# Performance work log

Hardware: AMD Instinct MI355X
Metric: run time of the kernel (lower is better)

## Reference

```python
import jax, jax.numpy as jnp
import numpy as np

N = 6144
M_VID = 1024
M_AUD = 128
APPERTURE = 20
EPS = 1e-6


def setup_inputs() -> dict:
    key = jax.random.key(0)
    ks = jax.random.split(key, 16)
    s = 0.02
    inp = {
        "x": jax.random.normal(ks[0], (1, N, M_VID), dtype=jnp.float32),
        "x_audio": jax.random.normal(ks[1], (1, N, M_AUD), dtype=jnp.float32),
        "seq_len": N,
        "audio_len": N,
        # video self-attention (torch Linear convention: W is [out, in])
        "Wk_v": jax.random.normal(ks[2], (M_VID, M_VID), dtype=jnp.float32) * s,
        "Wq_v": jax.random.normal(ks[3], (M_VID, M_VID), dtype=jnp.float32) * s,
        "Wv_v": jax.random.normal(ks[4], (M_VID, M_VID), dtype=jnp.float32) * s,
        "Wo_v": jax.random.normal(ks[5], (M_VID, M_VID), dtype=jnp.float32) * s,
        # audio self-attention
        "Wk_a": jax.random.normal(ks[6], (M_AUD, M_AUD), dtype=jnp.float32) * s,
        "Wq_a": jax.random.normal(ks[7], (M_AUD, M_AUD), dtype=jnp.float32) * s,
        "Wv_a": jax.random.normal(ks[8], (M_AUD, M_AUD), dtype=jnp.float32) * s,
        "Wo_a": jax.random.normal(ks[9], (M_AUD, M_AUD), dtype=jnp.float32) * s,
        # MLP head
        "ka_w": jax.random.normal(ks[10], (1024, M_VID + M_AUD), dtype=jnp.float32) * s,
        "ka_b": jnp.zeros((1024,), dtype=jnp.float32),
        "kd_w": jax.random.normal(ks[11], (1, 1024), dtype=jnp.float32) * s,
        "kd_b": jnp.zeros((1,), dtype=jnp.float32),
        # layer norms
        "ln_y_g": jnp.ones((M_VID,), dtype=jnp.float32),
        "ln_y_b": jnp.zeros((M_VID,), dtype=jnp.float32),
        "ln_ya_g": jnp.ones((M_AUD,), dtype=jnp.float32),
        "ln_ya_b": jnp.zeros((M_AUD,), dtype=jnp.float32),
        "ln_ka_g": jnp.ones((1024,), dtype=jnp.float32),
        "ln_ka_b": jnp.zeros((1024,), dtype=jnp.float32),
    }
    return inp


def _layer_norm(x, g, b):
    mu = jnp.mean(x, axis=-1, keepdims=True)
    var = jnp.mean((x - mu) ** 2, axis=-1, keepdims=True)
    return (x - mu) / jnp.sqrt(var + EPS) * g + b


def _self_attention(x, Wk, Wq, Wv, Wo):
    # x: [N, d]
    n = x.shape[0]
    K = x @ Wk.T
    Q = (x @ Wq.T) * 0.06
    V = x @ Wv.T
    logits = Q @ K.T  # [N, N]
    # keep only |i-j| < apperture (trimask masks |i-j| >= apperture)
    idx = jnp.arange(n)
    band = jnp.abs(idx[:, None] - idx[None, :]) < APPERTURE
    logits = jnp.where(band, logits, -jnp.inf)
    att = jax.nn.softmax(logits, axis=-1)  # [N, N]
    # torch: y = (V^T @ att)^T == att^T @ V  (note the transpose on att!)
    y = att.T @ V
    return y @ Wo.T, att


def reference(x, x_audio, seq_len, audio_len,
              Wk_v, Wq_v, Wv_v, Wo_v,
              Wk_a, Wq_a, Wv_a, Wo_a,
              ka_w, ka_b, kd_w, kd_b,
              ln_y_g, ln_y_b, ln_ya_g, ln_ya_b, ln_ka_g, ln_ka_b):
    m = x.shape[2]
    m_audio = x_audio.shape[2]
    xf = x.reshape(-1, m)            # [N, 1024]
    xa = x_audio.reshape(-1, m_audio)  # [N, 128]

    y, att_w = _self_attention(xf, Wk_v, Wq_v, Wv_v, Wo_v)
    y = _layer_norm(y + xf, ln_y_g, ln_y_b)

    ya, att_wa = _self_attention(xa, Wk_a, Wq_a, Wv_a, Wo_a)
    ya = _layer_norm(ya + xa, ln_ya_g, ln_ya_b)

    y_comb = jnp.concatenate((y, ya), axis=1)        # [N, 1152]
    att_comb = jnp.concatenate((att_w, att_wa), axis=1)  # [N, 2N]

    h = jax.nn.relu(y_comb @ ka_w.T + ka_b)
    h = _layer_norm(h, ln_ka_g, ln_ka_b)
    score = jax.nn.sigmoid(h @ kd_w.T + kd_b)  # [N, 1]
    score = score.reshape(1, -1)               # [1, N]
    return score, att_comb
```

## Files before the change

kernel.cpp:

```cpp
#include <hip/hip_runtime.h>
#include <stdint.h>

typedef unsigned short u16;
typedef unsigned int u32;
typedef __attribute__((ext_vector_type(8))) short bf16x8;
typedef __attribute__((ext_vector_type(4))) short s16x4;
typedef __attribute__((ext_vector_type(4))) float f32x4;
typedef __attribute__((ext_vector_type(2))) float f32x2;

#define DEV __device__ __forceinline__

DEV u16 f2bf(float f) {
  union { float f; unsigned u; } v; v.f = f;
  unsigned r = v.u + 0x7fffu + ((v.u >> 16) & 1u);
  return (u16)(r >> 16);
}
DEV float bf2f(u16 h) {
  union { u32 u; float f; } v; v.u = ((u32)h) << 16; return v.f;
}
DEV float lo16(u32 w) { union { u32 u; float f; } v; v.u = w << 16; return v.f; }
DEV float hi16(u32 w) { union { u32 u; float f; } v; v.u = w & 0xFFFF0000u; return v.f; }
DEV int imax(int a, int b) { return a > b ? a : b; }
DEV int imin(int a, int b) { return a < b ? a : b; }

DEV int xcd_swz(int b0, int nwg) {
  int q = nwg >> 3, r = nwg & 7, x = b0 & 7, l = b0 >> 3;
  return (x < r ? x * (q + 1) : r * (q + 1) + (x - r) * q) + l;
}

DEV void g2lds16(const u16* g, u16* l) {
  __builtin_amdgcn_global_load_lds(
      (const __attribute__((address_space(1))) void*)g,
      (__attribute__((address_space(3))) void*)l, 16, 0, 0);
}

#define NSEG 5
struct CastTab {
  const float* src[NSEG];
  u16* dst[NSEG];
  int start[NSEG + 1];
};
struct TransTab {
  const float* src[6];
  u16* dst[6];
  int n[6];
  int start[7];
};

__global__ __launch_bounds__(256) void vas_prep(CastTab t, int total4,
                                                int castBlocks, TransTab tt) {
  if ((int)blockIdx.x < castBlocks) {
    int idx = blockIdx.x * 256 + threadIdx.x;
    if (idx >= total4) return;
    int s = 0;
#pragma unroll
    for (int k = 1; k < NSEG; ++k)
      if (idx >= t.start[k]) s = k;
    int local = idx - t.start[s];
    f32x4 f = ((const f32x4*)t.src[s])[local];
    s16x4 o;
    o.x = (short)f2bf(f.x);
    o.y = (short)f2bf(f.y);
    o.z = (short)f2bf(f.z);
    o.w = (short)f2bf(f.w);
    ((s16x4*)t.dst[s])[local] = o;
  } else {
    __shared__ float tl[32][33];
    int b = blockIdx.x - castBlocks;
    int s = 0;
#pragma unroll
    for (int k = 1; k < 6; ++k)
      if (b >= tt.start[k]) s = k;
    b -= tt.start[s];
    const float* src = tt.src[s];
    u16* dst = tt.dst[s];
    const int n = tt.n[s];
    const int tpr = n >> 5;
    const int tr = (b / tpr) * 32, tc = (b % tpr) * 32;
    const int lx = threadIdx.x & 31, ly = threadIdx.x >> 5;
#pragma unroll
    for (int r = 0; r < 4; ++r)
      tl[ly + r * 8][lx] = src[(size_t)(tr + ly + r * 8) * n + tc + lx];
    __syncthreads();
#pragma unroll
    for (int r = 0; r < 4; ++r)
      dst[(size_t)(tc + ly + r * 8) * n + tr + lx] = f2bf(tl[lx][ly + r * 8]);
  }
}

struct GemmP {
  const u16* A;
  const u16* W;
  void* C;
  const float* bias;
  int M, Nn, K, mode;
};

__global__ __launch_bounds__(256) void vas_gemm4(
    GemmP p0, GemmP p1, GemmP p2, GemmP p3, int s1, int s2, int s3) {
  const int bs = xcd_swz(blockIdx.x, gridDim.x);

  GemmP p;
  int bid;
  if (bs < s1) { p = p0; bid = bs; }
  else if (bs < s2) { p = p1; bid = bs - s1; }
  else if (bs < s3) { p = p2; bid = bs - s2; }
  else { p = p3; bid = bs - s3; }

  __shared__ u16 As[2][128 * 32];
  __shared__ u16 Ws[2][128 * 32];
  const int tid = threadIdx.x;
  const int lane = tid & 63;
  const int wave = tid >> 6;

  const int Mb = p.M >> 7, Nb = p.Nn >> 7;
  const int GM = 8;
  int per = GM * Nb;
  int g = bid / per;
  int rem = bid - g * per;
  int gm = imin(GM, Mb - g * GM);
  int mblk = g * GM + rem % gm;
  int nblk = rem / gm;
  const int m0 = mblk * 128;
  const int n0 = nblk * 128;
  const int wm = (wave >> 1) * 64;
  const int wn = (wave & 1) * 64;

  const int smat = wave >> 1;
  const int skh = wave & 1;
  const u16* ssrc = smat ? p.W : p.A;
  const int sbase = smat ? n0 : m0;
  u16* sdstBase = (smat ? &Ws[skh][0] : &As[skh][0]) + lane * 8;
  const int srow = lane >> 2;
  const int scol = (lane & 3) * 8;

  f32x4 acc[4][4] = {};

  for (int k0 = 0; k0 < p.K; k0 += 64) {
#pragma unroll
    for (int u = 0; u < 8; ++u) {
      int r0 = u * 16;
      g2lds16(ssrc + (size_t)(sbase + r0 + srow) * p.K + (k0 + skh * 32 + scol),
              sdstBase + r0 * 32);
    }
    __syncthreads();
#pragma unroll
    for (int kk = 0; kk < 2; ++kk) {
      bf16x8 af[4], bfr[4];
#pragma unroll
      for (int t = 0; t < 4; ++t)
        af[t] = *(const bf16x8*)(&As[kk][0] + (wm + t * 16 + (lane & 15)) * 32 + (lane >> 4) * 8);
#pragma unroll
      for (int t = 0; t < 4; ++t)
        bfr[t] = *(const bf16x8*)(&Ws[kk][0] + (wn + t * 16 + (lane & 15)) * 32 + (lane >> 4) * 8);
#pragma unroll
      for (int mi = 0; mi < 4; ++mi)
#pragma unroll
        for (int ni = 0; ni < 4; ++ni)
          acc[mi][ni] = __builtin_amdgcn_mfma_f32_16x16x32_bf16(af[mi], bfr[ni], acc[mi][ni], 0, 0, 0);
    }
    __syncthreads();
  }

#pragma unroll
  for (int mi = 0; mi < 4; ++mi) {
#pragma unroll
    for (int ni = 0; ni < 4; ++ni) {
      int col = n0 + wn + ni * 16 + (lane & 15);
      float bv = p.bias ? p.bias[col] : 0.f;
#pragma unroll
      for (int r = 0; r < 4; ++r) {
        int row = m0 + wm + mi * 16 + (lane >> 4) * 4 + r;
        float vv = acc[mi][ni][r] + bv;
        size_t idx = (size_t)row * p.Nn + col;
        if (p.mode == 0) ((float*)p.C)[idx] = vv;
        else if (p.mode == 1) ((u16*)p.C)[idx] = f2bf(fmaxf(vv, 0.f));
        else ((u16*)p.C)[idx] = f2bf(vv);
      }
    }
  }
}

__global__ __launch_bounds__(256) void vas_battn(
    const u16* __restrict__ Xv, const u16* __restrict__ Xa,
    const u16* __restrict__ KKVv, const u16* __restrict__ KKVa,
    float* __restrict__ bandV, float* __restrict__ bandA,
    float* __restrict__ attBase, int N, float scale, int vb) {
  const int lane = threadIdx.x & 63;
  const int wave = threadIdx.x >> 6;
  const bool video = blockIdx.x < (u32)vb;
  const int i = (video ? blockIdx.x : blockIdx.x - vb) * 4 + wave;
  const int lo = imax(i - 19, 0);
  const int hi = imin(i + 19, N - 1);
  const int nj = hi - lo + 1;
  float logit = 0.f;
  __shared__ float a_sh[4][40];

  if (video) {
    float qf[16];
    const u16* qrow = Xv + (size_t)i * 1024;
#pragma unroll
    for (int c = 0; c < 2; ++c) {
      bf16x8 qv = *(const bf16x8*)(qrow + c * 512 + lane * 8);
      const u32* qw = (const u32*)&qv;
#pragma unroll
      for (int t = 0; t < 4; ++t) {
        qf[c * 8 + 2 * t] = lo16(qw[t]);
        qf[c * 8 + 2 * t + 1] = hi16(qw[t]);
      }
    }
#pragma unroll 2
    for (int s = 0; s < nj; ++s) {
      const u16* kr = KKVv + (size_t)(lo + s) * 2048;
      float p = 0.f;
#pragma unroll
      for (int c = 0; c < 2; ++c) {
        bf16x8 kv = *(const bf16x8*)(kr + c * 512 + lane * 8);
        const u32* kw = (const u32*)&kv;
#pragma unroll
        for (int t = 0; t < 4; ++t)
          p += lo16(kw[t]) * qf[c * 8 + 2 * t] + hi16(kw[t]) * qf[c * 8 + 2 * t + 1];
      }
#pragma unroll
      for (int off = 32; off; off >>= 1) p += __shfl_xor(p, off);
      if (lane == s) logit = p;
    }
  } else {
    u32 q = *(const u32*)(Xa + (size_t)i * 128 + lane * 2);
    float q0 = lo16(q), q1 = hi16(q);
#pragma unroll 2
    for (int s = 0; s < nj; ++s) {
      u32 k = *(const u32*)(KKVa + (size_t)(lo + s) * 256 + lane * 2);
      float p = lo16(k) * q0 + hi16(k) * q1;
#pragma unroll
      for (int off = 32; off; off >>= 1) p += __shfl_xor(p, off);
      if (lane == s) logit = p;
    }
  }

  logit *= scale;
  float v = (lane < nj) ? logit : -3.4e38f;
  float mx = v;
#pragma unroll
  for (int off = 32; off; off >>= 1) mx = fmaxf(mx, __shfl_xor(mx, off));
  float e = (lane < nj) ? __expf(v - mx) : 0.f;
  float den = e;
#pragma unroll
  for (int off = 32; off; off >>= 1) den += __shfl_xor(den, off);
  float att = (lane < nj) ? e / den : 0.f;
  float* band = video ? bandV : bandA;
  if (lane < 40) {
    band[i * 40 + lane] = att;
    a_sh[wave][lane] = att;
  }

  f32x4* rowp = (f32x4*)(attBase + (size_t)i * 2 * N + (video ? 0 : N));
  const int nchunks = N / 4;
  const int cLo = lo >> 2, cHi = hi >> 2;
  for (int c = lane; c < nchunks; c += 64) {
    f32x4 o = {0.f, 0.f, 0.f, 0.f};
    if (c >= cLo && c <= cHi) {
      int col0 = c * 4;
#pragma unroll
      for (int e2 = 0; e2 < 4; ++e2) {
        int col = col0 + e2;
        if (col >= lo && col <= hi) o[e2] = a_sh[wave][col - lo];
      }
    }
    __builtin_nontemporal_store(o, &rowp[c]);
  }
}

#define JT 8
__global__ __launch_bounds__(256) void vas_apply_ln(
    const u16* __restrict__ KKVv, const u16* __restrict__ KKVa,
    const float* __restrict__ bandV, const float* __restrict__ bandA,
    const float* __restrict__ Xv, const float* __restrict__ Xa,
    const float* __restrict__ gv, const float* __restrict__ bv_,
    const float* __restrict__ ga, const float* __restrict__ ba,
    u16* __restrict__ out, int outStride, int N, int vb) {
  const int tid = threadIdx.x;
  __shared__ float a_sh[(JT + 38) * JT];
  __shared__ float red[2][JT][4];

  if (blockIdx.x < (u32)vb) {
    const int j0 = blockIdx.x * JT;
    const int base = j0 - 19;
    for (int idx = tid; idx < (JT + 38) * JT; idx += 256) {
      int s = idx / JT, jj = idx % JT;
      int i = base + s;
      int j = j0 + jj;
      float w = 0.f;
      if (i >= 0 && i < N) {
        int d = j - i;
        if (d > -20 && d < 20) w = bandV[i * 40 + (j - imax(i - 19, 0))];
      }
      a_sh[s * JT + jj] = w;
    }
    __syncthreads();

    f32x4 acc[JT] = {};
    const int sLo = imax(0, -base);
    const int sHi = imin(JT + 38, N - base);
    s16x4 nxt = *(const s16x4*)(KKVv + (size_t)(base + sLo) * 2048 + 1024 + tid * 4);
    for (int s = sLo; s < sHi; ++s) {
      s16x4 raw = nxt;
      if (s + 1 < sHi)
        nxt = *(const s16x4*)(KKVv + (size_t)(base + s + 1) * 2048 + 1024 + tid * 4);
      f32x4 vv;
      vv.x = bf2f((u16)raw.x);
      vv.y = bf2f((u16)raw.y);
      vv.z = bf2f((u16)raw.z);
      vv.w = bf2f((u16)raw.w);
#pragma unroll
      for (int jj = 0; jj < JT; ++jj) {
        float a = a_sh[s * JT + jj];
        acc[jj].x += a * vv.x;
        acc[jj].y += a * vv.y;
        acc[jj].z += a * vv.z;
        acc[jj].w += a * vv.w;
      }
    }

    const int lane = tid & 63, wave = tid >> 6;
#pragma unroll
    for (int jj = 0; jj < JT; ++jj) {
      f32x4 x4 = ((const f32x4*)(Xv + (size_t)(j0 + jj) * 1024))[tid];
      f32x4 v;
      v.x = acc[jj].x + x4.x;
      v.y = acc[jj].y + x4.y;
      v.z = acc[jj].z + x4.z;
      v.w = acc[jj].w + x4.w;
      acc[jj] = v;
      float s = v.x + v.y + v.z + v.w;
      float s2 = v.x * v.x + v.y * v.y + v.z * v.z + v.w * v.w;
#pragma unroll
      for (int off = 32; off; off >>= 1) {
        s += __shfl_xor(s, off);
        s2 += __shfl_xor(s2, off);
      }
      if (lane == 0) { red[0][jj][wave] = s; red[1][jj][wave] = s2; }
    }
    __syncthreads();
    f32x4 gg = ((const f32x4*)gv)[tid];
    f32x4 bb = ((const f32x4*)bv_)[tid];
#pragma unroll
    for (int jj = 0; jj < JT; ++jj) {
      float S = red[0][jj][0] + red[0][jj][1] + red[0][jj][2] + red[0][jj][3];
      float S2 = red[1][jj][0] + red[1][jj][1] + red[1][jj][2] + red[1][jj][3];
      float mu = S / 1024.f;
      float var = S2 / 1024.f - mu * mu;
      float inv = rsqrtf(var + 1e-6f);
      f32x4 v = acc[jj];
      s16x4 o;
      o.x = (short)f2bf((v.x - mu) * inv * gg.x + bb.x);
      o.y = (short)f2bf((v.y - mu) * inv * gg.y + bb.y);
      o.z = (short)f2bf((v.z - mu) * inv * gg.z + bb.z);
      o.w = (short)f2bf((v.w - mu) * inv * gg.w + bb.w);
      *(s16x4*)(out + (size_t)(j0 + jj) * outStride + tid * 4) = o;
    }
  } else {
    const int lane = tid & 63;
    const int wave = tid >> 6;
    const int j = (blockIdx.x - vb) * 4 + wave;
    const int lo = imax(j - 19, 0);
    const int hi = imin(j + 19, N - 1);
    const int ni = hi - lo + 1;
    float* aw = a_sh + wave * 40;
    if (lane < ni) {
      int i = lo + lane;
      aw[lane] = bandA[i * 40 + (j - imax(i - 19, 0))];
    }
    __syncthreads();
    f32x2 acc = {0.f, 0.f};
#pragma unroll 4
    for (int s = 0; s < ni; ++s) {
      float a = aw[s];
      u32 k = *(const u32*)(KKVa + (size_t)(lo + s) * 256 + 128 + lane * 2);
      acc.x += a * lo16(k);
      acc.y += a * hi16(k);
    }
    f32x2 x2 = *(const f32x2*)(Xa + (size_t)j * 128 + lane * 2);
    float vx = acc.x + x2.x;
    float vy = acc.y + x2.y;
    float s = vx + vy, s2 = vx * vx + vy * vy;
#pragma unroll
    for (int off = 32; off; off >>= 1) {
      s += __shfl_xor(s, off);
      s2 += __shfl_xor(s2, off);
    }
    float mu = s / 128.f;
    float var = s2 / 128.f - mu * mu;
    float inv = rsqrtf(var + 1e-6f);
    f32x2 g2 = *(const f32x2*)(ga + lane * 2);
    f32x2 b2 = *(const f32x2*)(ba + lane * 2);
    u32 o = (u32)f2bf((vx - mu) * inv * g2.x + b2.x) |
            ((u32)f2bf((vy - mu) * inv * g2.y + b2.y) << 16);
    *(u32*)(out + (size_t)j * outStride + 1024 + lane * 2) = o;
  }
}

__global__ __launch_bounds__(256) void vas_head(
    const u16* __restrict__ H, const float* __restrict__ g,
    const float* __restrict__ bb, const float* __restrict__ kw,
    const float* __restrict__ kb, float* __restrict__ score) {
  const int row = blockIdx.x;
  const int tid = threadIdx.x, lane = tid & 63, wave = tid >> 6;
  __shared__ float shA[4], shB[4];
  s16x4 raw = ((const s16x4*)(H + (size_t)row * 1024))[tid];
  f32x4 v;
  v.x = bf2f((u16)raw.x);
  v.y = bf2f((u16)raw.y);
  v.z = bf2f((u16)raw.z);
  v.w = bf2f((u16)raw.w);
  float s = v.x + v.y + v.z + v.w;
  float s2 = v.x * v.x + v.y * v.y + v.z * v.z + v.w * v.w;
#pragma unroll
  for (int off = 32; off; off >>= 1) {
    s += __shfl_xor(s, off);
    s2 += __shfl_xor(s2, off);
  }
  if (lane == 0) { shA[wave] = s; shB[wave] = s2; }
  __syncthreads();
  float S = shA[0] + shA[1] + shA[2] + shA[3];
  float S2 = shB[0] + shB[1] + shB[2] + shB[3];
  float mu = S / 1024.f;
  float var = S2 / 1024.f - mu * mu;
  float inv = rsqrtf(var + 1e-6f);
  f32x4 gg = ((const f32x4*)g)[tid];
  f32x4 bv = ((const f32x4*)bb)[tid];
  f32x4 kv = ((const f32x4*)kw)[tid];
  float p = ((v.x - mu) * inv * gg.x + bv.x) * kv.x +
            ((v.y - mu) * inv * gg.y + bv.y) * kv.y +
            ((v.z - mu) * inv * gg.z + bv.z) * kv.z +
            ((v.w - mu) * inv * gg.w + bv.w) * kv.w;
#pragma unroll
  for (int off = 32; off; off >>= 1) p += __shfl_xor(p, off);
  __syncthreads();
  if (lane == 0) shA[wave] = p;
  __syncthreads();
  if (tid == 0) {
    float P = shA[0] + shA[1] + shA[2] + shA[3] + kb[0];
    score[row] = 1.f / (1.f + __expf(-P));
  }
}

extern "C" void kernel_launch(void* const* d_in, const int* in_sizes, int n_in,
                              void* d_out, int out_size, void* d_ws, size_t ws_size,
                              hipStream_t stream) {
  const float* x = (const float*)d_in[0];
  const float* xa = (const float*)d_in[1];
  const float* Wk_v = (const float*)d_in[4];
  const float* Wq_v = (const float*)d_in[5];
  const float* Wv_v = (const float*)d_in[6];
  const float* Wo_v = (const float*)d_in[7];
  const float* Wk_a = (const float*)d_in[8];
  const float* Wq_a = (const float*)d_in[9];
  const float* Wv_a = (const float*)d_in[10];
  const float* Wo_a = (const float*)d_in[11];
  const float* ka_w = (const float*)d_in[12];
  const float* ka_b = (const float*)d_in[13];
  const float* kd_w = (const float*)d_in[14];
  const float* kd_b = (const float*)d_in[15];
  const float* ln_y_g = (const float*)d_in[16];
  const float* ln_y_b = (const float*)d_in[17];
  const float* ln_ya_g = (const float*)d_in[18];
  const float* ln_ya_b = (const float*)d_in[19];
  const float* ln_ka_g = (const float*)d_in[20];
  const float* ln_ka_b = (const float*)d_in[21];

  const int N = in_sizes[0] / 1024;
  const int MV = 1024, MA = 128, MH = 1152;

  char* wsb = (char*)d_ws;
  size_t off = 0;
  auto alloc = [&](size_t bytes) -> void* {
    void* p = wsb + off;
    off += (bytes + 255) & ~(size_t)255;
    return p;
  };
  u16* xf_b   = (u16*)alloc((size_t)N * MV * 2);
  u16* xa_b   = (u16*)alloc((size_t)N * MA * 2);
  u16* wov_b  = (u16*)alloc((size_t)MV * MV * 2);
  u16* woa_b  = (u16*)alloc((size_t)MA * MA * 2);
  u16* wqTv   = (u16*)alloc((size_t)MV * MV * 2);
  u16* wkTv   = (u16*)alloc((size_t)MV * MV * 2);
  u16* wvTv   = (u16*)alloc((size_t)MV * MV * 2);
  u16* wqTa   = (u16*)alloc((size_t)MA * MA * 2);
  u16* wkTa   = (u16*)alloc((size_t)MA * MA * 2);
  u16* wvTa   = (u16*)alloc((size_t)MA * MA * 2);
  u16* wWv    = (u16*)alloc((size_t)2 * MV * MV * 2);
  u16* wWa    = (u16*)alloc((size_t)2 * MA * MA * 2);
  u16* kaw_b  = (u16*)alloc((size_t)1024 * MH * 2);
  u16* KKVv   = (u16*)alloc((size_t)N * 2 * MV * 2);
  u16* KKVa   = (u16*)alloc((size_t)N * 2 * MA * 2);
  float* bandV = (float*)alloc((size_t)N * 40 * 4);
  float* bandA = (float*)alloc((size_t)N * 40 * 4);
  u16* ycomb_b = (u16*)alloc((size_t)N * MH * 2);
  u16* h_b = (u16*)alloc((size_t)N * 1024 * 2);

  float* dout = (float*)d_out;
  float* attBase = dout + N;

  {
    CastTab t;
    int c = 0, cum = 0;
    auto seg = [&](const float* s, u16* d, size_t n) {
      t.src[c] = s; t.dst[c] = d; t.start[c] = cum; cum += (int)(n / 4); ++c;
    };
    seg(x, xf_b, (size_t)N * MV);
    seg(xa, xa_b, (size_t)N * MA);
    seg(Wo_v, wov_b, (size_t)MV * MV);
    seg(Wo_a, woa_b, (size_t)MA * MA);
    seg(ka_w, kaw_b, (size_t)1024 * MH);
    t.start[c] = cum;
    int castBlocks = (cum + 255) / 256;

    TransTab tt;
    int c2 = 0, cum2 = 0;
    auto seg2 = [&](const float* s, u16* d, int n) {
      tt.src[c2] = s; tt.dst[c2] = d; tt.n[c2] = n; tt.start[c2] = cum2;
      cum2 += (n / 32) * (n / 32); ++c2;
    };
    seg2(Wq_v, wqTv, MV);
    seg2(Wk_v, wkTv, MV);
    seg2(Wv_v, wvTv, MV);
    seg2(Wq_a, wqTa, MA);
    seg2(Wk_a, wkTa, MA);
    seg2(Wv_a, wvTa, MA);
    tt.start[c2] = cum2;

    vas_prep<<<castBlocks + cum2, 256, 0, stream>>>(t, cum, castBlocks, tt);
  }

  {
    GemmP gv = {wqTv, wkTv, wWv, nullptr, MV, MV, MV, 2};
    GemmP uv = {wov_b, wvTv, wWv + (size_t)MV * MV, nullptr, MV, MV, MV, 2};
    GemmP ga = {wqTa, wkTa, wWa, nullptr, MA, MA, MA, 2};
    GemmP ua = {woa_b, wvTa, wWa + (size_t)MA * MA, nullptr, MA, MA, MA, 2};
    int bg = (MV / 128) * (MV / 128);
    vas_gemm4<<<2 * bg + 2, 256, 0, stream>>>(gv, uv, ga, ua, bg, 2 * bg, 2 * bg + 1);
  }

  {
    GemmP pv = {xf_b, wWv, KKVv, nullptr, N, 2 * MV, MV, 2};
    GemmP pa = {xa_b, wWa, KKVa, nullptr, N, 2 * MA, MA, 2};
    int bv = (N / 128) * (2 * MV / 128);
    int ba = (N / 128) * (2 * MA / 128);
    vas_gemm4<<<bv + ba, 256, 0, stream>>>(pv, pa, pa, pa, bv, bv + ba, bv + ba);
  }

  vas_battn<<<N / 2, 256, 0, stream>>>(xf_b, xa_b, KKVv, KKVa, bandV, bandA,
                                       attBase, N, 0.06f, N / 4);

  vas_apply_ln<<<N / JT + N / 4, 256, 0, stream>>>(
      KKVv, KKVa, bandV, bandA, x, xa,
      ln_y_g, ln_y_b, ln_ya_g, ln_ya_b, ycomb_b, MH, N, N / JT);

  {
    GemmP ph = {ycomb_b, kaw_b, h_b, ka_b, N, 1024, MH, 1};
    int bh = (N / 128) * (1024 / 128);
    vas_gemm4<<<bh, 256, 0, stream>>>(ph, ph, ph, ph, bh, bh, bh);
  }

  vas_head<<<N, 256, 0, stream>>>(h_b, ln_ka_g, ln_ka_b, kd_w, kd_b, dout);
}
```

Before: 558.7 us.

## Fuse head LayerNorm and score dot-product into the MLP GEMM epilogue

The head GEMM no longer writes the N×1024 bf16 hidden activation. Its epilogue applies ReLU and reduces per-row partial sums of h, h², and h·(kd_w·gamma) per 128-column tile into a small partial buffer. A tiny score kernel combines the 8 partials per row and applies LayerNorm algebraically (mean/variance plus precomputed gamma and beta dot products) before the sigmoid. This removes a 12 MB write/read round trip and a 6144-block kernel. In exchange it adds shared-memory reductions in the GEMM epilogue and uses the single-pass variance formula in fp32 rather than bf16-rounded h.

```diff
diff --git a/kernel.cpp b/kernel.cpp
--- a/kernel.cpp
+++ b/kernel.cpp
@@ -181,6 +181,147 @@
   }
 }
 
+__global__ __launch_bounds__(256) void vas_gemmh(
+    GemmP p, const float* __restrict__ kw, const float* __restrict__ gw,
+    float* __restrict__ part) {
+  const int bid = xcd_swz(blockIdx.x, gridDim.x);
+
+  __shared__ u16 As[2][128 * 32];
+  __shared__ u16 Ws[2][128 * 32];
+  __shared__ float hp[2][128][3];
+  const int tid = threadIdx.x;
+  const int lane = tid & 63;
+  const int wave = tid >> 6;
+
+  const int Mb = p.M >> 7, Nb = p.Nn >> 7;
+  const int GM = 8;
+  int per = GM * Nb;
+  int g = bid / per;
+  int rem = bid - g * per;
+  int gm = imin(GM, Mb - g * GM);
+  int mblk = g * GM + rem % gm;
+  int nblk = rem / gm;
+  const int m0 = mblk * 128;
+  const int n0 = nblk * 128;
+  const int wm = (wave >> 1) * 64;
+  const int wn = (wave & 1) * 64;
+
+  const int smat = wave >> 1;
+  const int skh = wave & 1;
+  const u16* ssrc = smat ? p.W : p.A;
+  const int sbase = smat ? n0 : m0;
+  u16* sdstBase = (smat ? &Ws[skh][0] : &As[skh][0]) + lane * 8;
+  const int srow = lane >> 2;
+  const int scol = (lane & 3) * 8;
+
+  f32x4 acc[4][4] = {};
+
+  for (int k0 = 0; k0 < p.K; k0 += 64) {
+#pragma unroll
+    for (int u = 0; u < 8; ++u) {
+      int r0 = u * 16;
+      g2lds16(ssrc + (size_t)(sbase + r0 + srow) * p.K + (k0 + skh * 32 + scol),
+              sdstBase + r0 * 32);
+    }
+    __syncthreads();
+#pragma unroll
+    for (int kk = 0; kk < 2; ++kk) {
+      bf16x8 af[4], bfr[4];
+#pragma unroll
+      for (int t = 0; t < 4; ++t)
+        af[t] = *(const bf16x8*)(&As[kk][0] + (wm + t * 16 + (lane & 15)) * 32 + (lane >> 4) * 8);
+#pragma unroll
+      for (int t = 0; t < 4; ++t)
+        bfr[t] = *(const bf16x8*)(&Ws[kk][0] + (wn + t * 16 + (lane & 15)) * 32 + (lane >> 4) * 8);
+#pragma unroll
+      for (int mi = 0; mi < 4; ++mi)
+#pragma unroll
+        for (int ni = 0; ni < 4; ++ni)
+          acc[mi][ni] = __builtin_amdgcn_mfma_f32_16x16x32_bf16(af[mi], bfr[ni], acc[mi][ni], 0, 0, 0);
+    }
+    __syncthreads();
+  }
+
+  float kwg[4], bb[4];
+#pragma unroll
+  for (int ni = 0; ni < 4; ++ni) {
+    int col = n0 + wn + ni * 16 + (lane & 15);
+    kwg[ni] = kw[col] * gw[col];
+    bb[ni] = p.bias ? p.bias[col] : 0.f;
+  }
+#pragma unroll
+  for (int mi = 0; mi < 4; ++mi) {
+#pragma unroll
+    for (int r = 0; r < 4; ++r) {
+      float s1 = 0.f, s2 = 0.f, dd = 0.f;
+#pragma unroll
+      for (int ni = 0; ni < 4; ++ni) {
+        float vv = fmaxf(acc[mi][ni][r] + bb[ni], 0.f);
+        s1 += vv;
+        s2 += vv * vv;
+        dd += vv * kwg[ni];
+      }
+#pragma unroll
+      for (int off = 1; off < 16; off <<= 1) {
+        s1 += __shfl_xor(s1, off);
+        s2 += __shfl_xor(s2, off);
+        dd += __shfl_xor(dd, off);
+      }
+      if ((lane & 15) == 0) {
+        int row = wm + mi * 16 + (lane >> 4) * 4 + r;
+        hp[wave & 1][row][0] = s1;
+        hp[wave & 1][row][1] = s2;
+        hp[wave & 1][row][2] = dd;
+      }
+    }
+  }
+  __syncthreads();
+  if (tid < 128) {
+    float* pp = part + ((size_t)(m0 + tid) * 8 + nblk) * 3;
+    pp[0] = hp[0][tid][0] + hp[1][tid][0];
+    pp[1] = hp[0][tid][1] + hp[1][tid][1];
+    pp[2] = hp[0][tid][2] + hp[1][tid][2];
+  }
+}
+
+__global__ __launch_bounds__(256) void vas_score(
+    const float* __restrict__ part, const float* __restrict__ kw,
+    const float* __restrict__ g, const float* __restrict__ b,
+    const float* __restrict__ kb, float* __restrict__ score, int N) {
+  const int tid = threadIdx.x, lane = tid & 63, wave = tid >> 6;
+  __shared__ float shc[2][4];
+  f32x4 kv = ((const f32x4*)kw)[tid];
+  f32x4 gv = ((const f32x4*)g)[tid];
+  f32x4 bv = ((const f32x4*)b)[tid];
+  float c1 = kv.x * gv.x + kv.y * gv.y + kv.z * gv.z + kv.w * gv.w;
+  float c2 = kv.x * bv.x + kv.y * bv.y + kv.z * bv.z + kv.w * bv.w;
+#pragma unroll
+  for (int off = 32; off; off >>= 1) {
+    c1 += __shfl_xor(c1, off);
+    c2 += __shfl_xor(c2, off);
+  }
+  if (lane == 0) { shc[0][wave] = c1; shc[1][wave] = c2; }
+  __syncthreads();
+  float C1 = shc[0][0] + shc[0][1] + shc[0][2] + shc[0][3];
+  float C2 = shc[1][0] + shc[1][1] + shc[1][2] + shc[1][3];
+  int row = blockIdx.x * 256 + tid;
+  if (row < N) {
+    const float* pp = part + (size_t)row * 24;
+    float s1 = 0.f, s2 = 0.f, dd = 0.f;
+#pragma unroll
+    for (int k = 0; k < 8; ++k) {
+      s1 += pp[k * 3];
+      s2 += pp[k * 3 + 1];
+      dd += pp[k * 3 + 2];
+    }
+    float mu = s1 / 1024.f;
+    float var = s2 / 1024.f - mu * mu;
+    float inv = rsqrtf(var + 1e-6f);
+    float P = inv * dd - inv * mu * C1 + C2 + kb[0];
+    score[row] = 1.f / (1.f + __expf(-P));
+  }
+}
+
 __global__ __launch_bounds__(256) void vas_battn(
     const u16* __restrict__ Xv, const u16* __restrict__ Xa,
     const u16* __restrict__ KKVv, const u16* __restrict__ KKVa,
@@ -397,51 +538,6 @@
     u32 o = (u32)f2bf((vx - mu) * inv * g2.x + b2.x) |
             ((u32)f2bf((vy - mu) * inv * g2.y + b2.y) << 16);
     *(u32*)(out + (size_t)j * outStride + 1024 + lane * 2) = o;
-  }
-}
-
-__global__ __launch_bounds__(256) void vas_head(
-    const u16* __restrict__ H, const float* __restrict__ g,
-    const float* __restrict__ bb, const float* __restrict__ kw,
-    const float* __restrict__ kb, float* __restrict__ score) {
-  const int row = blockIdx.x;
-  const int tid = threadIdx.x, lane = tid & 63, wave = tid >> 6;
-  __shared__ float shA[4], shB[4];
-  s16x4 raw = ((const s16x4*)(H + (size_t)row * 1024))[tid];
-  f32x4 v;
-  v.x = bf2f((u16)raw.x);
-  v.y = bf2f((u16)raw.y);
-  v.z = bf2f((u16)raw.z);
-  v.w = bf2f((u16)raw.w);
-  float s = v.x + v.y + v.z + v.w;
-  float s2 = v.x * v.x + v.y * v.y + v.z * v.z + v.w * v.w;
-#pragma unroll
-  for (int off = 32; off; off >>= 1) {
-    s += __shfl_xor(s, off);
-    s2 += __shfl_xor(s2, off);
-  }
-  if (lane == 0) { shA[wave] = s; shB[wave] = s2; }
-  __syncthreads();
-  float S = shA[0] + shA[1] + shA[2] + shA[3];
-  float S2 = shB[0] + shB[1] + shB[2] + shB[3];
-  float mu = S / 1024.f;
-  float var = S2 / 1024.f - mu * mu;
-  float inv = rsqrtf(var + 1e-6f);
-  f32x4 gg = ((const f32x4*)g)[tid];
-  f32x4 bv = ((const f32x4*)bb)[tid];
-  f32x4 kv = ((const f32x4*)kw)[tid];
-  float p = ((v.x - mu) * inv * gg.x + bv.x) * kv.x +
-            ((v.y - mu) * inv * gg.y + bv.y) * kv.y +
-            ((v.z - mu) * inv * gg.z + bv.z) * kv.z +
-            ((v.w - mu) * inv * gg.w + bv.w) * kv.w;
-#pragma unroll
-  for (int off = 32; off; off >>= 1) p += __shfl_xor(p, off);
-  __syncthreads();
-  if (lane == 0) shA[wave] = p;
-  __syncthreads();
-  if (tid == 0) {
-    float P = shA[0] + shA[1] + shA[2] + shA[3] + kb[0];
-    score[row] = 1.f / (1.f + __expf(-P));
   }
 }
 
@@ -497,7 +593,7 @@
   float* bandV = (float*)alloc((size_t)N * 40 * 4);
   float* bandA = (float*)alloc((size_t)N * 40 * 4);
   u16* ycomb_b = (u16*)alloc((size_t)N * MH * 2);
-  u16* h_b = (u16*)alloc((size_t)N * 1024 * 2);
+  float* part_b = (float*)alloc((size_t)N * 8 * 3 * 4);
 
   float* dout = (float*)d_out;
   float* attBase = dout + N;
@@ -558,10 +654,11 @@
       ln_y_g, ln_y_b, ln_ya_g, ln_ya_b, ycomb_b, MH, N, N / JT);
 
   {
-    GemmP ph = {ycomb_b, kaw_b, h_b, ka_b, N, 1024, MH, 1};
+    GemmP ph = {ycomb_b, kaw_b, nullptr, ka_b, N, 1024, MH, 1};
     int bh = (N / 128) * (1024 / 128);
-    vas_gemm4<<<bh, 256, 0, stream>>>(ph, ph, ph, ph, bh, bh, bh);
-  }
-
-  vas_head<<<N, 256, 0, stream>>>(h_b, ln_ka_g, ln_ka_b, kd_w, kd_b, dout);
-}
+    vas_gemmh<<<bh, 256, 0, stream>>>(ph, kd_w, ln_ka_g, part_b);
+  }
+
+  vas_score<<<(N + 255) / 256, 256, 0, stream>>>(
+      part_b, kd_w, ln_ka_g, ln_ka_b, kd_b, dout, N);
+}
```

After: 551.1 us. No clear change (-1.4%).
